# Performance work log

Measured on AMD Instinct MI355X. Metric: run time of the kernel, lower is better.

## Reference

```python
import jax, jax.numpy as jnp
import numpy as np

N_NODES = 50000
IN_FEAT = 256
UNITS = 256
N_EDGES = 800000


def setup_inputs() -> dict:
    key = jax.random.key(0)
    k1, k2, k3, k4, k5 = jax.random.split(key, 5)
    x = jax.random.normal(k1, (N_NODES, IN_FEAT), dtype=jnp.float32)
    # glorot_uniform-style weight
    limit = float(np.sqrt(6.0 / (IN_FEAT + UNITS)))
    w = jax.random.uniform(k2, (IN_FEAT, UNITS), dtype=jnp.float32, minval=-limit, maxval=limit)
    # COO sparse adjacency (e.g. symmetrically-normalized GCN adjacency values)
    adj_vals = jax.random.uniform(k3, (N_EDGES,), dtype=jnp.float32)
    adj_rows = jax.random.randint(k4, (N_EDGES,), 0, N_NODES, dtype=jnp.int32)
    adj_cols = jax.random.randint(k5, (N_EDGES,), 0, N_NODES, dtype=jnp.int32)
    return {"x": x, "w": w, "adj_vals": adj_vals, "adj_rows": adj_rows, "adj_cols": adj_cols}


def reference(x, w, adj_vals, adj_rows, adj_cols):
    # dropout rate = 0.0 -> identity
    h = jnp.matmul(x, w)                       # [N, units] dense projection
    # SpMM: out[r] = sum_e vals[e] * h[cols[e]] for edges with rows[e] == r
    msg = adj_vals[:, None] * h[adj_cols]      # [E, units] gathered messages
    out = jax.ops.segment_sum(msg, adj_rows, num_segments=N_NODES)  # [N, units]
    return jax.nn.relu(out)
```

## Files before the change

kernel.cpp:

```cpp
#include <hip/hip_runtime.h>

#define N_NODES 50000
#define N_EDGES 800000
#define CAP     48

typedef __bf16 v8bf __attribute__((ext_vector_type(8)));
typedef float  v4f  __attribute__((ext_vector_type(4)));

__device__ __forceinline__ float bf2f(ushort u) {
    return __uint_as_float(((unsigned int)u) << 16);
}
__device__ __forceinline__ ushort f2bf(float f) {
    unsigned int u = __float_as_uint(f);
    u += 0x7FFFu + ((u >> 16) & 1u);
    return (ushort)(u >> 16);
}

__global__ __launch_bounds__(256) void k_prep(const void* __restrict__ Wv,
                                              const int* __restrict__ rows,
                                              const int* __restrict__ cols,
                                              const void* __restrict__ valsv,
                                              int* __restrict__ flag,
                                              int* __restrict__ counts,
                                              ushort* __restrict__ WTB,
                                              uint* __restrict__ erec) {
    const int b = blockIdx.x, t = threadIdx.x;
    __shared__ int det;
    __shared__ ushort sW[32][258];

    if (b < 8) {
        if (t == 0) det = 0;
        __syncthreads();
        {
            ushort u = ((const ushort*)Wv)[t * 2];
            if (fabsf(bf2f(u)) > 0.2f) atomicAdd(&det, 1);
        }
        __syncthreads();
        const bool isf32 = (det > 8);
        if (t == 0 && det) atomicAdd(flag, det);

        for (int kk = 0; kk < 32; ++kk) {
            int k = b * 32 + kk;
            ushort v;
            if (isf32) v = f2bf(((const float*)Wv)[k * 256 + t]);
            else       v = ((const ushort*)Wv)[k * 256 + t];
            sW[kk][t] = v;
        }
        __syncthreads();
        ushort tmp[32];
        #pragma unroll
        for (int kk = 0; kk < 32; ++kk) tmp[kk] = sW[kk][t];
        uint4* dst = (uint4*)(WTB + b * 8192 + t * 32);
        #pragma unroll
        for (int c = 0; c < 4; ++c) {
            const ushort* p = &tmp[c * 8];
            uint4 v;
            v.x = (uint)p[0] | ((uint)p[1] << 16);
            v.y = (uint)p[2] | ((uint)p[3] << 16);
            v.z = (uint)p[4] | ((uint)p[5] << 16);
            v.w = (uint)p[6] | ((uint)p[7] << 16);
            dst[c] = v;
        }
        return;
    }

    if (t == 0) det = 0;
    __syncthreads();
    {
        ushort u = ((const ushort*)valsv)[t * 2];
        if (fabsf(bf2f(u)) > 1.5f) atomicAdd(&det, 1);
    }
    __syncthreads();
    const bool isf32 = (det > 8);

    const int e = (b - 8) * 256 + t;
    int r = rows[e];
    int p = atomicAdd(&counts[r], 1);
    if (p < CAP) {
        ushort v;
        if (isf32) v = f2bf(((const float*)valsv)[e]);
        else       v = ((const ushort*)valsv)[e];
        uint rec = (uint)(ushort)cols[e] | ((uint)v << 16);
        __builtin_nontemporal_store(rec, &erec[r * CAP + p]);
    }
}

#define ASTRIDE 264
__global__ __launch_bounds__(256) void k_fused(const void* __restrict__ Xv,
                                               const uint* __restrict__ erec,
                                               const int* __restrict__ counts,
                                               const ushort* __restrict__ WTB,
                                               const int* __restrict__ flag,
                                               void* __restrict__ Out) {
    bool isf32 = (*flag > 100);
    __shared__ __align__(16) ushort sA[32 * ASTRIDE];
    const int t = threadIdx.x;
    const int lane = t & 63, wv = t >> 6;
    const int mBase = blockIdx.x * 32;

    const int f = lane * 4;
    for (int lr = 0; lr < 8; ++lr) {
        const int rloc = wv * 8 + lr;
        const int r = mBase + rloc;
        const int start = r * CAP;
        const int cnt   = (r < N_NODES) ? min(counts[r], CAP) : 0;
        float a0 = 0.f, a1 = 0.f, a2 = 0.f, a3 = 0.f;
        const int nbatch = (cnt + 7) >> 3;
        if (isf32) {
            const float* Xf = (const float*)Xv;
            for (int bb = 0; bb < nbatch; ++bb) {
                int j0 = bb * 8;
                int cc[8]; float vv[8];
                #pragma unroll
                for (int i = 0; i < 8; ++i) {
                    int jj = j0 + i;
                    uint m = erec[start + (jj < cnt ? jj : cnt - 1)];
                    cc[i] = (int)(m & 0xFFFFu);
                    vv[i] = (jj < cnt) ? bf2f((ushort)(m >> 16)) : 0.f;
                }
                float4 g[8];
                #pragma unroll
                for (int i = 0; i < 8; ++i)
                    g[i] = *(const float4*)(Xf + (size_t)cc[i] * 256 + f);
                #pragma unroll
                for (int i = 0; i < 8; ++i) {
                    float v = vv[i];
                    a0 = fmaf(v, g[i].x, a0); a1 = fmaf(v, g[i].y, a1);
                    a2 = fmaf(v, g[i].z, a2); a3 = fmaf(v, g[i].w, a3);
                }
            }
        } else {
            const ushort* Xb = (const ushort*)Xv;
            for (int bb = 0; bb < nbatch; ++bb) {
                int j0 = bb * 8;
                int cc[8]; float vv[8];
                #pragma unroll
                for (int i = 0; i < 8; ++i) {
                    int jj = j0 + i;
                    uint m = erec[start + (jj < cnt ? jj : cnt - 1)];
                    cc[i] = (int)(m & 0xFFFFu);
                    vv[i] = (jj < cnt) ? bf2f((ushort)(m >> 16)) : 0.f;
                }
                ushort4 g[8];
                #pragma unroll
                for (int i = 0; i < 8; ++i)
                    g[i] = *(const ushort4*)(Xb + (size_t)cc[i] * 256 + f);
                #pragma unroll
                for (int i = 0; i < 8; ++i) {
                    float v = vv[i];
                    a0 = fmaf(v, bf2f(g[i].x), a0); a1 = fmaf(v, bf2f(g[i].y), a1);
                    a2 = fmaf(v, bf2f(g[i].z), a2); a3 = fmaf(v, bf2f(g[i].w), a3);
                }
            }
        }
        ushort4 o;
        o.x = f2bf(a0); o.y = f2bf(a1); o.z = f2bf(a2); o.w = f2bf(a3);
        *(ushort4*)&sA[rloc * ASTRIDE + f] = o;
    }
    __syncthreads();

    const int fr = lane & 15, q = lane >> 4;
    v4f acc[2][4] = {};
    for (int kc = 0; kc < 8; ++kc) {
        v8bf a0 = *(const v8bf*)&sA[(fr)      * ASTRIDE + kc * 32 + q * 8];
        v8bf a1 = *(const v8bf*)&sA[(16 + fr) * ASTRIDE + kc * 32 + q * 8];
        #pragma unroll
        for (int j = 0; j < 4; ++j) {
            int n = wv * 64 + j * 16 + fr;
            v8bf bfr = *(const v8bf*)(WTB + kc * 8192 + n * 32 + q * 8);
            acc[0][j] = __builtin_amdgcn_mfma_f32_16x16x32_bf16(a0, bfr, acc[0][j], 0, 0, 0);
            acc[1][j] = __builtin_amdgcn_mfma_f32_16x16x32_bf16(a1, bfr, acc[1][j], 0, 0, 0);
        }
    }

    #pragma unroll
    for (int mt = 0; mt < 2; ++mt) {
        #pragma unroll
        for (int j = 0; j < 4; ++j) {
            #pragma unroll
            for (int rr = 0; rr < 4; ++rr) {
                int grow = mBase + mt * 16 + q * 4 + rr;
                if (grow < N_NODES) {
                    int gcol = wv * 64 + j * 16 + fr;
                    float v = fmaxf(acc[mt][j][rr], 0.f);
                    if (isf32) __builtin_nontemporal_store(v, (float*)Out + (size_t)grow * 256 + gcol);
                    else       __builtin_nontemporal_store(f2bf(v), (ushort*)Out + (size_t)grow * 256 + gcol);
                }
            }
        }
    }
}

#define OFF_FLAG   ((size_t)0)
#define OFF_CNT    ((size_t)256)
#define OFF_WTB    ((size_t)200512)
#define OFF_EREC   ((size_t)331584)

extern "C" void kernel_launch(void* const* d_in, const int* in_sizes, int n_in,
                              void* d_out, int out_size, void* d_ws, size_t ws_size,
                              hipStream_t stream) {
    const void* X    = d_in[0];
    const void* W    = d_in[1];
    const void* VALS = d_in[2];
    const int*  ROWS = (const int*)d_in[3];
    const int*  COLS = (const int*)d_in[4];

    char* ws = (char*)d_ws;
    int*    flag   = (int*)(ws + OFF_FLAG);
    int*    counts = (int*)(ws + OFF_CNT);
    ushort* WTB    = (ushort*)(ws + OFF_WTB);
    uint*   erec   = (uint*)(ws + OFF_EREC);

    hipMemsetAsync(ws, 0, 200512, stream);

    k_prep<<<8 + N_EDGES / 256, 256, 0, stream>>>(W, ROWS, COLS, VALS, flag, counts, WTB, erec);
    k_fused<<<(N_NODES + 31) / 32, 256, 0, stream>>>(X, erec, counts, WTB, flag, d_out);
}
```

Before: 273.2 us.

## Vectorize edge bucketing and halve rows per block in fused kernel

The prep kernel now has each thread handle four edges with int4/float4 loads, issuing four atomics per thread and using ordinary stores instead of nontemporal stores for the edge records. The fused gather+MFMA kernel processes 16 rows per block instead of 32, which doubles the grid, halves shared memory, and drops the bounds checks because 50000 is divisible by 16. The intent is fewer, wider loads in the prep pass and more blocks for latency hiding in the gather. In exchange, each block reloads the W tile from global memory for only half the rows, so that traffic doubles.

```diff
diff --git a/kernel.cpp b/kernel.cpp
--- a/kernel.cpp
+++ b/kernel.cpp
@@ -73,15 +73,37 @@
     __syncthreads();
     const bool isf32 = (det > 8);
 
-    const int e = (b - 8) * 256 + t;
-    int r = rows[e];
-    int p = atomicAdd(&counts[r], 1);
-    if (p < CAP) {
-        ushort v;
-        if (isf32) v = f2bf(((const float*)valsv)[e]);
-        else       v = ((const ushort*)valsv)[e];
-        uint rec = (uint)(ushort)cols[e] | ((uint)v << 16);
-        __builtin_nontemporal_store(rec, &erec[r * CAP + p]);
+    const int e0 = (b - 8) * 1024 + t * 4;
+    if (e0 + 3 < N_EDGES) {
+        int4 r4 = *(const int4*)(rows + e0);
+        int4 c4 = *(const int4*)(cols + e0);
+        ushort v0, v1, v2, v3;
+        if (isf32) {
+            float4 f4 = *(const float4*)((const float*)valsv + e0);
+            v0 = f2bf(f4.x); v1 = f2bf(f4.y); v2 = f2bf(f4.z); v3 = f2bf(f4.w);
+        } else {
+            ushort4 u4 = *(const ushort4*)((const ushort*)valsv + e0);
+            v0 = u4.x; v1 = u4.y; v2 = u4.z; v3 = u4.w;
+        }
+        int p0 = atomicAdd(&counts[r4.x], 1);
+        int p1 = atomicAdd(&counts[r4.y], 1);
+        int p2 = atomicAdd(&counts[r4.z], 1);
+        int p3 = atomicAdd(&counts[r4.w], 1);
+        if (p0 < CAP) erec[r4.x * CAP + p0] = (uint)(ushort)c4.x | ((uint)v0 << 16);
+        if (p1 < CAP) erec[r4.y * CAP + p1] = (uint)(ushort)c4.y | ((uint)v1 << 16);
+        if (p2 < CAP) erec[r4.z * CAP + p2] = (uint)(ushort)c4.z | ((uint)v2 << 16);
+        if (p3 < CAP) erec[r4.w * CAP + p3] = (uint)(ushort)c4.w | ((uint)v3 << 16);
+    } else {
+        for (int e = e0; e < N_EDGES; ++e) {
+            int r = rows[e];
+            int p = atomicAdd(&counts[r], 1);
+            if (p < CAP) {
+                ushort v;
+                if (isf32) v = f2bf(((const float*)valsv)[e]);
+                else       v = ((const ushort*)valsv)[e];
+                erec[r * CAP + p] = (uint)(ushort)cols[e] | ((uint)v << 16);
+            }
+        }
     }
 }
 
@@ -93,23 +115,23 @@
                                                const int* __restrict__ flag,
                                                void* __restrict__ Out) {
     bool isf32 = (*flag > 100);
-    __shared__ __align__(16) ushort sA[32 * ASTRIDE];
+    __shared__ __align__(16) ushort sA[16 * ASTRIDE];
     const int t = threadIdx.x;
     const int lane = t & 63, wv = t >> 6;
-    const int mBase = blockIdx.x * 32;
+    const int mBase = blockIdx.x * 16;
 
     const int f = lane * 4;
-    for (int lr = 0; lr < 8; ++lr) {
-        const int rloc = wv * 8 + lr;
+    for (int lr = 0; lr < 4; ++lr) {
+        const int rloc = wv * 4 + lr;
         const int r = mBase + rloc;
         const int start = r * CAP;
-        const int cnt   = (r < N_NODES) ? min(counts[r], CAP) : 0;
+        const int cnt   = min(counts[r], CAP);
         float a0 = 0.f, a1 = 0.f, a2 = 0.f, a3 = 0.f;
         const int nbatch = (cnt + 7) >> 3;
         if (isf32) {
             const float* Xf = (const float*)Xv;
-            for (int bb = 0; bb < nbatch; ++bb) {
-                int j0 = bb * 8;
+            for (int b = 0; b < nbatch; ++b) {
+                int j0 = b * 8;
                 int cc[8]; float vv[8];
                 #pragma unroll
                 for (int i = 0; i < 8; ++i) {
@@ -131,8 +153,8 @@
             }
         } else {
             const ushort* Xb = (const ushort*)Xv;
-            for (int bb = 0; bb < nbatch; ++bb) {
-                int j0 = bb * 8;
+            for (int b = 0; b < nbatch; ++b) {
+                int j0 = b * 8;
                 int cc[8]; float vv[8];
                 #pragma unroll
                 for (int i = 0; i < 8; ++i) {
@@ -160,33 +182,26 @@
     __syncthreads();
 
     const int fr = lane & 15, q = lane >> 4;
-    v4f acc[2][4] = {};
+    v4f acc[4] = {};
     for (int kc = 0; kc < 8; ++kc) {
-        v8bf a0 = *(const v8bf*)&sA[(fr)      * ASTRIDE + kc * 32 + q * 8];
-        v8bf a1 = *(const v8bf*)&sA[(16 + fr) * ASTRIDE + kc * 32 + q * 8];
+        v8bf a = *(const v8bf*)&sA[fr * ASTRIDE + kc * 32 + q * 8];
         #pragma unroll
         for (int j = 0; j < 4; ++j) {
             int n = wv * 64 + j * 16 + fr;
-            v8bf bfr = *(const v8bf*)(WTB + kc * 8192 + n * 32 + q * 8);
-            acc[0][j] = __builtin_amdgcn_mfma_f32_16x16x32_bf16(a0, bfr, acc[0][j], 0, 0, 0);
-            acc[1][j] = __builtin_amdgcn_mfma_f32_16x16x32_bf16(a1, bfr, acc[1][j], 0, 0, 0);
+            v8bf b = *(const v8bf*)(WTB + kc * 8192 + n * 32 + q * 8);
+            acc[j] = __builtin_amdgcn_mfma_f32_16x16x32_bf16(a, b, acc[j], 0, 0, 0);
         }
     }
 
     #pragma unroll
-    for (int mt = 0; mt < 2; ++mt) {
-        #pragma unroll
-        for (int j = 0; j < 4; ++j) {
-            #pragma unroll
-            for (int rr = 0; rr < 4; ++rr) {
-                int grow = mBase + mt * 16 + q * 4 + rr;
-                if (grow < N_NODES) {
-                    int gcol = wv * 64 + j * 16 + fr;
-                    float v = fmaxf(acc[mt][j][rr], 0.f);
-                    if (isf32) __builtin_nontemporal_store(v, (float*)Out + (size_t)grow * 256 + gcol);
-                    else       __builtin_nontemporal_store(f2bf(v), (ushort*)Out + (size_t)grow * 256 + gcol);
-                }
-            }
+    for (int j = 0; j < 4; ++j) {
+        #pragma unroll
+        for (int rr = 0; rr < 4; ++rr) {
+            int grow = mBase + q * 4 + rr;
+            int gcol = wv * 64 + j * 16 + fr;
+            float v = fmaxf(acc[j][rr], 0.f);
+            if (isf32) __builtin_nontemporal_store(v, (float*)Out + (size_t)grow * 256 + gcol);
+            else       __builtin_nontemporal_store(f2bf(v), (ushort*)Out + (size_t)grow * 256 + gcol);
         }
     }
 }
@@ -213,6 +228,7 @@
 
     hipMemsetAsync(ws, 0, 200512, stream);
 
-    k_prep<<<8 + N_EDGES / 256, 256, 0, stream>>>(W, ROWS, COLS, VALS, flag, counts, WTB, erec);
-    k_fused<<<(N_NODES + 31) / 32, 256, 0, stream>>>(X, erec, counts, WTB, flag, d_out);
-}
+    k_prep<<<8 + (N_EDGES + 1023) / 1024, 256, 0, stream>>>(W, ROWS, COLS, VALS,
+                                                            flag, counts, WTB, erec);
+    k_fused<<<N_NODES / 16, 256, 0, stream>>>(X, erec, counts, WTB, flag, d_out);
+}
```

Measured after the change: 269.5 us. Within noise of the previous version (-1.4%).
